# Kernel optimization log

Hardware: AMD Instinct MI355X
Metric: run time of the kernel (lower is better)

## Reference

```python
import jax, jax.numpy as jnp
import numpy as np

B, S, D, H = 4, 4096, 1024, 16
DH = D // H


def setup_inputs() -> dict:
    key = jax.random.key(0)
    ks = jax.random.split(key, 8)
    scale = 1.0 / np.sqrt(D)
    return {
        "q": jax.random.normal(ks[0], (B, S, D), jnp.float32),
        "k": jax.random.normal(ks[1], (B, S, D), jnp.float32),
        "v": jax.random.normal(ks[2], (B, S, D), jnp.float32),
        "mask": jax.random.uniform(ks[3], (H, H), jnp.float32),
        # torch nn.Linear weights, layout [out, in]; applied as x @ W.T
        "Wq": jax.random.normal(ks[4], (D, D), jnp.float32) * scale,
        "Wk": jax.random.normal(ks[5], (D, D), jnp.float32) * scale,
        "Wv": jax.random.normal(ks[6], (D, D), jnp.float32) * scale,
        "Wo": jax.random.normal(ks[7], (D, D), jnp.float32) * scale,
    }


def reference(q, k, v, mask, Wq, Wk, Wv, Wo):
    # projections (bias-free Linear): x @ W.T, then split to [B,S,H,DH]
    qh = (q @ Wq.T).reshape(B, S, H, DH)
    kh = (k @ Wk.T).reshape(B, S, H, DH)
    vh = (v @ Wv.T).reshape(B, S, H, DH)
    # Faithful to source: NO head/seq transpose, so attention is over the
    # head axis per token: score [B,S,H,H]
    score = jnp.einsum('bshd,bsgd->bshg', qh, kh) / np.sqrt(DH)
    score = score * mask  # multiplicative mask, broadcast [H,H]
    p = jax.nn.softmax(score, axis=-1)
    attn = jnp.einsum('bshg,bsgd->bshd', p, vh)  # [B,S,H,DH]
    out = attn.reshape(B, S, D) @ Wo.T
    return out
```

## Files before the change

### kernel.cpp

```cpp
#include <hip/hip_runtime.h>
#include <hip/hip_bf16.h>
#include <stdint.h>


namespace {
constexpr int kD  = 1024;
constexpr int kH  = 16;
constexpr int kDH = 64;
constexpr int kM  = 4 * 4096;
constexpr size_t PER = (size_t)kM * kD;
constexpr size_t WSZ = (size_t)kD * kD;

typedef __attribute__((ext_vector_type(4))) float f32x4;
typedef __attribute__((ext_vector_type(8))) short s16x8;

__device__ __forceinline__ unsigned short f2b(float f) {
  uint32_t x = __builtin_bit_cast(uint32_t, f);
  x += 0x7fffu + ((x >> 16) & 1u);
  return (unsigned short)(x >> 16);
}
__device__ __forceinline__ float b2f(unsigned short u) {
  return __builtin_bit_cast(float, (uint32_t)u << 16);
}

typedef __attribute__((address_space(3))) void as3_void;
typedef __attribute__((address_space(1))) void as1_void;
__device__ __forceinline__ void gload_lds16(const void* g, void* l) {
  __builtin_amdgcn_global_load_lds((const as1_void*)(uintptr_t)g,
                                   (as3_void*)(uint32_t)(uintptr_t)l, 16, 0, 0);
}

__global__ __launch_bounds__(256) void cvt_bf16(
    const float* __restrict__ q, const float* __restrict__ k, const float* __restrict__ v,
    const float* __restrict__ Wq, const float* __restrict__ Wk, const float* __restrict__ Wv,
    const float* __restrict__ Wo, unsigned short* __restrict__ out) {
  const size_t total8 = (3 * PER + 4 * WSZ) / 8;
  for (size_t i8 = (size_t)blockIdx.x * blockDim.x + threadIdx.x; i8 < total8;
       i8 += (size_t)gridDim.x * blockDim.x) {
    size_t i = i8 * 8;
    const float* s; size_t o;
    if (i < 3 * PER) {
      if (i < PER)            { s = q; o = i; }
      else if (i < 2 * PER)   { s = k; o = i - PER; }
      else                    { s = v; o = i - 2 * PER; }
    } else {
      size_t j = i - 3 * PER;
      if (j < WSZ)            { s = Wq; o = j; }
      else if (j < 2 * WSZ)   { s = Wk; o = j - WSZ; }
      else if (j < 3 * WSZ)   { s = Wv; o = j - 2 * WSZ; }
      else                    { s = Wo; o = j - 3 * WSZ; }
    }
    f32x4 f0 = ((const f32x4*)(s + o))[0];
    f32x4 f1 = ((const f32x4*)(s + o))[1];
    s16x8 r;
#pragma unroll
    for (int d = 0; d < 4; ++d) {
      r[d]     = (short)f2b(f0[d]);
      r[4 + d] = (short)f2b(f1[d]);
    }
    *(s16x8*)(out + i) = r;
  }
}

constexpr int BM2 = 256, BN2 = 256, BK2 = 64;
constexpr int KT2 = kD / BK2;

__device__ __forceinline__ void mfma16(f32x4 (&a)[2][4], s16x8 (&af)[2][2],
                                       s16x8 (&bw)[4][2]) {
  __builtin_amdgcn_s_setprio(1);
#pragma unroll
  for (int mi = 0; mi < 2; ++mi)
#pragma unroll
    for (int nj = 0; nj < 4; ++nj)
#pragma unroll
      for (int kk = 0; kk < 2; ++kk)
        a[mi][nj] = __builtin_amdgcn_mfma_f32_16x16x32_bf16(af[mi][kk], bw[nj][kk],
                                                            a[mi][nj], 0, 0, 0);
  __builtin_amdgcn_s_setprio(0);
}

template <bool OUT_F32>
__device__ __forceinline__ void gemmq_body(const unsigned short* __restrict__ A,
                                           const unsigned short* __restrict__ Bm,
                                           void* __restrict__ Cp) {
  constexpr int K = kD, N = kD;
  __shared__ __align__(16) unsigned short lds[65536];

  const int lin = blockIdx.y * gridDim.x + blockIdx.x;
  const int xcd = lin & 7;
  const int idx = lin >> 3;
  const int m0 = (xcd * 8 + (idx >> 2)) * BM2;
  const int n0 = (idx & 3) * BN2;

  const int t    = threadIdx.x;
  const int lane = t & 63;
  const int w    = t >> 6;
  const int wrow = w >> 1;
  const int wcol = w & 1;

  const int srow  = lane >> 3;
  const int sslot = (lane & 7) ^ srow;
  const int fr     = lane & 15;
  const int fkslot = lane >> 4;

  auto stageHalf = [&](const unsigned short* src, int grow0, int k0, int slot) {
    const unsigned short* g = src + (size_t)(grow0 + w * 16 + srow) * K + k0 + sslot * 8;
    unsigned short* l = lds + slot * 8192 + w * 16 * 64;
    gload_lds16(g, l);
    gload_lds16(g + (size_t)8 * K, l + 8 * 64);
  };
  auto rdA = [&](int slot, int mi, int kk) -> s16x8 {
    int r = wrow * 32 + mi * 16 + fr;
    int s16 = (kk * 4 + fkslot) ^ (r & 7);
    return *(const s16x8*)(lds + slot * 8192 + r * 64 + s16 * 8);
  };
  auto rdB = [&](int slot, int nj, int kk) -> s16x8 {
    int r = wcol * 64 + nj * 16 + fr;
    int s16 = (kk * 4 + fkslot) ^ (r & 7);
    return *(const s16x8*)(lds + slot * 8192 + r * 64 + s16 * 8);
  };

  f32x4 acc[4][2][4];
#pragma unroll
  for (int qi = 0; qi < 4; ++qi)
#pragma unroll
    for (int mi = 0; mi < 2; ++mi)
#pragma unroll
      for (int nj = 0; nj < 4; ++nj) acc[qi][mi][nj] = (f32x4){0.f, 0.f, 0.f, 0.f};

  stageHalf(A,  m0,       0, 0);
  stageHalf(Bm, n0,       0, 2);
  stageHalf(A,  m0 + 128, 0, 1);
  stageHalf(Bm, n0 + 128, 0, 3);

  s16x8 af[2][2], bw[4][2];

  for (int tt = 0; tt < KT2; ++tt) {
    const int b    = (tt & 1) * 4;
    const int nb   = b ^ 4;
    const int k1   = (tt + 1) * BK2;
    const bool more = (tt + 1 < KT2);

    asm volatile("s_waitcnt vmcnt(0)" ::: "memory");
    asm volatile("s_barrier" ::: "memory");
    if (more) { stageHalf(A, m0, k1, nb + 0); stageHalf(Bm, n0, k1, nb + 2); }
#pragma unroll
    for (int mi = 0; mi < 2; ++mi)
#pragma unroll
      for (int kk = 0; kk < 2; ++kk) af[mi][kk] = rdA(b + 0, mi, kk);
#pragma unroll
    for (int nj = 0; nj < 4; ++nj)
#pragma unroll
      for (int kk = 0; kk < 2; ++kk) bw[nj][kk] = rdB(b + 2, nj, kk);
    mfma16(acc[0], af, bw);

    asm volatile("s_barrier" ::: "memory");
    if (more) stageHalf(A, m0 + 128, k1, nb + 1);
#pragma unroll
    for (int mi = 0; mi < 2; ++mi)
#pragma unroll
      for (int kk = 0; kk < 2; ++kk) af[mi][kk] = rdA(b + 1, mi, kk);
    mfma16(acc[1], af, bw);

    asm volatile("s_barrier" ::: "memory");
    if (more) stageHalf(Bm, n0 + 128, k1, nb + 3);
#pragma unroll
    for (int nj = 0; nj < 4; ++nj)
#pragma unroll
      for (int kk = 0; kk < 2; ++kk) bw[nj][kk] = rdB(b + 3, nj, kk);
    mfma16(acc[2], af, bw);

    asm volatile("s_barrier" ::: "memory");
#pragma unroll
    for (int mi = 0; mi < 2; ++mi)
#pragma unroll
      for (int kk = 0; kk < 2; ++kk) af[mi][kk] = rdA(b + 0, mi, kk);
    mfma16(acc[3], af, bw);
  }

  constexpr int MH[4] = {0, 1, 1, 0};
  constexpr int NH[4] = {0, 0, 1, 1};
  const int cr = (lane >> 4) * 4;
  const int cc = lane & 15;
#pragma unroll
  for (int qi = 0; qi < 4; ++qi)
#pragma unroll
    for (int mi = 0; mi < 2; ++mi)
#pragma unroll
      for (int nj = 0; nj < 4; ++nj)
#pragma unroll
        for (int r = 0; r < 4; ++r) {
          size_t row = (size_t)(m0 + MH[qi] * 128 + wrow * 32 + mi * 16 + cr + r);
          size_t col = (size_t)(n0 + NH[qi] * 128 + wcol * 64 + nj * 16 + cc);
          if constexpr (OUT_F32)
            ((float*)Cp)[row * N + col] = acc[qi][mi][nj][r];
          else
            ((unsigned short*)Cp)[row * N + col] = f2b(acc[qi][mi][nj][r]);
        }
}

__global__ __launch_bounds__(512, 2) void proj_gemmq(
    const unsigned short* __restrict__ qb, const unsigned short* __restrict__ kb,
    const unsigned short* __restrict__ vb, const unsigned short* __restrict__ Wqb,
    const unsigned short* __restrict__ Wkb, const unsigned short* __restrict__ Wvb,
    unsigned short* __restrict__ qh, unsigned short* __restrict__ kh,
    unsigned short* __restrict__ vh) {
  const unsigned short *A, *W;
  unsigned short* C;
  if (blockIdx.z == 0)      { A = qb; W = Wqb; C = qh; }
  else if (blockIdx.z == 1) { A = kb; W = Wkb; C = kh; }
  else                      { A = vb; W = Wvb; C = vh; }
  gemmq_body<false>(A, W, C);
}

__global__ __launch_bounds__(512, 2) void out_gemmq(const unsigned short* __restrict__ attn,
                                                    const unsigned short* __restrict__ Wob,
                                                    float* __restrict__ out) {
  gemmq_body<true>(attn, Wob, out);
}

__global__ __launch_bounds__(256) void attn_tok(const unsigned short* __restrict__ qh,
                                                const unsigned short* __restrict__ kh,
                                                const unsigned short* __restrict__ vh,
                                                const float* __restrict__ mask,
                                                unsigned short* __restrict__ attn) {
  __shared__ float P[4][16][17];
  __shared__ __align__(16) unsigned short Vs[4][16 * 64];
  const int lane = threadIdx.x & 63;
  const int wid  = threadIdx.x >> 6;
  const size_t tok = (size_t)blockIdx.x * 4 + wid;

  const unsigned short* qp = qh + tok * kD;
  const unsigned short* kp = kh + tok * kD;
  const unsigned short* vp = vh + tok * kD;

  {
    const s16x8* src = (const s16x8*)vp;
    s16x8 a = src[2 * lane], b = src[2 * lane + 1];
    s16x8* dst = (s16x8*)Vs[wid];
    dst[2 * lane] = a;
    dst[2 * lane + 1] = b;
  }

  const int fr = lane & 15;
  const int fk = (lane >> 4) * 8;
  s16x8 a0 = *(const s16x8*)(qp + fr * kDH + fk);
  s16x8 a1 = *(const s16x8*)(qp + fr * kDH + 32 + fk);
  s16x8 b0 = *(const s16x8*)(kp + fr * kDH + fk);
  s16x8 b1 = *(const s16x8*)(kp + fr * kDH + 32 + fk);
  f32x4 s = {0.f, 0.f, 0.f, 0.f};
  s = __builtin_amdgcn_mfma_f32_16x16x32_bf16(a0, b0, s, 0, 0, 0);
  s = __builtin_amdgcn_mfma_f32_16x16x32_bf16(a1, b1, s, 0, 0, 0);

  const int cr = (lane >> 4) * 4;
  const int cc = lane & 15;
  float p[4];
#pragma unroll
  for (int r = 0; r < 4; ++r) {
    float val = s[r] * 0.125f * mask[(cr + r) * kH + cc];
    float mx = val;
#pragma unroll
    for (int d = 1; d < 16; d <<= 1) mx = fmaxf(mx, __shfl_xor(mx, d));
    float e = __expf(val - mx);
    float sum = e;
#pragma unroll
    for (int d = 1; d < 16; d <<= 1) sum += __shfl_xor(sum, d);
    p[r] = e / sum;
  }
#pragma unroll
  for (int r = 0; r < 4; ++r) P[wid][cr + r][cc] = p[r];

  const int h  = lane >> 2;
  const int d0 = (lane & 3) * 16;
  float o[16];
#pragma unroll
  for (int i = 0; i < 16; ++i) o[i] = 0.f;
#pragma unroll
  for (int g = 0; g < 16; ++g) {
    float pg = P[wid][h][g];
    s16x8 v0 = *(const s16x8*)(Vs[wid] + g * kDH + d0);
    s16x8 v1 = *(const s16x8*)(Vs[wid] + g * kDH + d0 + 8);
#pragma unroll
    for (int dd = 0; dd < 8; ++dd) {
      o[dd]     += pg * b2f((unsigned short)v0[dd]);
      o[8 + dd] += pg * b2f((unsigned short)v1[dd]);
    }
  }
  unsigned short* op = attn + tok * kD + h * kDH + d0;
  s16x8 r0, r1;
#pragma unroll
  for (int dd = 0; dd < 8; ++dd) {
    r0[dd] = (short)f2b(o[dd]);
    r1[dd] = (short)f2b(o[dd + 8]);
  }
  *(s16x8*)op = r0;
  *(s16x8*)(op + 8) = r1;
}

constexpr int BM = 128, BN = 128, BK = 32;
constexpr int LDSP = BK + 8;
__device__ __forceinline__ void cvt16_store(const float* __restrict__ g, short* __restrict__ l) {
  const f32x4* s4 = (const f32x4*)g;
  f32x4 f0 = s4[0], f1 = s4[1], f2 = s4[2], f3 = s4[3];
  s16x8 o0, o1;
#pragma unroll
  for (int i = 0; i < 4; ++i) {
    o0[i]     = (short)f2b(f0[i]);
    o0[4 + i] = (short)f2b(f1[i]);
    o1[i]     = (short)f2b(f2[i]);
    o1[4 + i] = (short)f2b(f3[i]);
  }
  *(s16x8*)l = o0;
  *(s16x8*)(l + 8) = o1;
}

template <bool A_BF16, bool OUT_F32>
__device__ __forceinline__ void gemm_body_cvt(const void* __restrict__ Ap,
                                              const float* __restrict__ Wp,
                                              void* __restrict__ Cp) {
  constexpr int N = kD, K = kD;
  __shared__ short As[BM * LDSP];
  __shared__ short Bs[BN * LDSP];
  const int t  = threadIdx.x;
  const int m0 = blockIdx.y * BM;
  const int n0 = blockIdx.x * BN;
  const int srow = t >> 1;
  const int scol = (t & 1) * 16;
  const int lane = t & 63;
  const int wid  = t >> 6;
  const int wm   = (wid >> 1) * 64;
  const int wn   = (wid & 1) * 64;
  const int fr   = lane & 15;
  const int fk   = (lane >> 4) * 8;

  f32x4 acc[4][4];
#pragma unroll
  for (int i = 0; i < 4; ++i)
#pragma unroll
    for (int j = 0; j < 4; ++j) acc[i][j] = (f32x4){0.f, 0.f, 0.f, 0.f};

  for (int k0 = 0; k0 < K; k0 += BK) {
    if constexpr (A_BF16) {
      const unsigned short* Ab = (const unsigned short*)Ap;
      const s16x8* src = (const s16x8*)(Ab + (size_t)(m0 + srow) * K + k0 + scol);
      s16x8 v0 = src[0], v1 = src[1];
      *(s16x8*)(As + srow * LDSP + scol) = v0;
      *(s16x8*)(As + srow * LDSP + scol + 8) = v1;
    } else {
      cvt16_store((const float*)Ap + (size_t)(m0 + srow) * K + k0 + scol,
                  As + srow * LDSP + scol);
    }
    cvt16_store(Wp + (size_t)(n0 + srow) * K + k0 + scol, Bs + srow * LDSP + scol);
    __syncthreads();
    s16x8 af[4], bw[4];
#pragma unroll
    for (int i = 0; i < 4; ++i)
      af[i] = *(const s16x8*)(As + (wm + i * 16 + fr) * LDSP + fk);
#pragma unroll
    for (int j = 0; j < 4; ++j)
      bw[j] = *(const s16x8*)(Bs + (wn + j * 16 + fr) * LDSP + fk);
#pragma unroll
    for (int i = 0; i < 4; ++i)
#pragma unroll
      for (int j = 0; j < 4; ++j)
        acc[i][j] = __builtin_amdgcn_mfma_f32_16x16x32_bf16(af[i], bw[j], acc[i][j], 0, 0, 0);
    __syncthreads();
  }
  const int cr = (lane >> 4) * 4;
  const int cc = lane & 15;
#pragma unroll
  for (int i = 0; i < 4; ++i)
#pragma unroll
    for (int j = 0; j < 4; ++j)
#pragma unroll
      for (int r = 0; r < 4; ++r) {
        size_t row = (size_t)(m0 + wm + i * 16 + cr + r);
        size_t col = (size_t)(n0 + wn + j * 16 + cc);
        if constexpr (OUT_F32)
          ((float*)Cp)[row * N + col] = acc[i][j][r];
        else
          ((unsigned short*)Cp)[row * N + col] = f2b(acc[i][j][r]);
      }
}

__global__ __launch_bounds__(256) void proj_gemm_cvt(
    const float* __restrict__ q, const float* __restrict__ k, const float* __restrict__ v,
    const float* __restrict__ Wq, const float* __restrict__ Wk, const float* __restrict__ Wv,
    unsigned short* __restrict__ qh, unsigned short* __restrict__ kh,
    unsigned short* __restrict__ vh) {
  const float* A; const float* W; unsigned short* C;
  if (blockIdx.z == 0)      { A = q; W = Wq; C = qh; }
  else if (blockIdx.z == 1) { A = k; W = Wk; C = kh; }
  else                      { A = v; W = Wv; C = vh; }
  gemm_body_cvt<false, false>(A, W, C);
}

__global__ __launch_bounds__(256) void out_gemm_cvt(const unsigned short* __restrict__ attn,
                                                    const float* __restrict__ Wo,
                                                    float* __restrict__ out) {
  gemm_body_cvt<true, true>(attn, Wo, out);
}

}

extern "C" void kernel_launch(void* const* d_in, const int* in_sizes, int n_in,
                              void* d_out, int out_size, void* d_ws, size_t ws_size,
                              hipStream_t stream) {
  (void)in_sizes; (void)n_in; (void)out_size;
  const float* q    = (const float*)d_in[0];
  const float* k    = (const float*)d_in[1];
  const float* v    = (const float*)d_in[2];
  const float* mask = (const float*)d_in[3];
  const float* Wq   = (const float*)d_in[4];
  const float* Wk   = (const float*)d_in[5];
  const float* Wv   = (const float*)d_in[6];
  const float* Wo   = (const float*)d_in[7];

  const size_t need = (6 * PER + 4 * WSZ) * sizeof(unsigned short);
  if (ws_size >= need) {
    unsigned short* qb  = (unsigned short*)d_ws;
    unsigned short* kb  = qb + PER;
    unsigned short* vb  = kb + PER;
    unsigned short* Wqb = vb + PER;
    unsigned short* Wkb = Wqb + WSZ;
    unsigned short* Wvb = Wkb + WSZ;
    unsigned short* Wob = Wvb + WSZ;
    unsigned short* qh  = Wob + WSZ;
    unsigned short* kh  = qh + PER;
    unsigned short* vh  = kh + PER;
    unsigned short* at  = qb;

    cvt_bf16<<<2048, 256, 0, stream>>>(q, k, v, Wq, Wk, Wv, Wo, qb);
    proj_gemmq<<<dim3(kD / BN2, kM / BM2, 3), 512, 0, stream>>>(qb, kb, vb, Wqb, Wkb, Wvb,
                                                                qh, kh, vh);
    attn_tok<<<dim3(kM / 4), 256, 0, stream>>>(qh, kh, vh, mask, at);
    out_gemmq<<<dim3(kD / BN2, kM / BM2), 512, 0, stream>>>(at, Wob, (float*)d_out);
  } else {
    unsigned short* qh = (unsigned short*)d_ws;
    unsigned short* kh = qh + PER;
    unsigned short* vh = kh + PER;
    unsigned short* at = (ws_size >= 4 * PER * sizeof(unsigned short)) ? (vh + PER) : qh;
    proj_gemm_cvt<<<dim3(kD / BN, kM / BM, 3), 256, 0, stream>>>(q, k, v, Wq, Wk, Wv,
                                                                 qh, kh, vh);
    attn_tok<<<dim3(kM / 4), 256, 0, stream>>>(qh, kh, vh, mask, at);
    out_gemm_cvt<<<dim3(kD / BN, kM / BM), 256, 0, stream>>>(at, Wo, (float*)d_out);
  }
}
```

Before: 227.8 us.

## Fuse fp32-to-bf16 activation conversion into projection GEMM A-tile staging

Removes the separate pass that converted q, k and v to bf16. The projection GEMM now loads fp32 A tiles into registers, converts them, and writes them swizzled into LDS, interleaved with the existing barrier phases; only the weights are still pre-converted, by a smaller kernel. This drops a large read-and-write pass over the activations and shrinks the workspace, and the attention output now reuses the qh buffer. The cost is that A staging moves from direct global-to-LDS loads to a register path, with more VGPR pressure, more global traffic per tile from fp32 rereads across column blocks, and an extra lgkmcnt wait per iteration.

```diff
diff --git a/kernel.cpp b/kernel.cpp
--- a/kernel.cpp
+++ b/kernel.cpp
@@ -30,26 +30,19 @@
                                    (as3_void*)(uint32_t)(uintptr_t)l, 16, 0, 0);
 }
 
-__global__ __launch_bounds__(256) void cvt_bf16(
-    const float* __restrict__ q, const float* __restrict__ k, const float* __restrict__ v,
-    const float* __restrict__ Wq, const float* __restrict__ Wk, const float* __restrict__ Wv,
-    const float* __restrict__ Wo, unsigned short* __restrict__ out) {
-  const size_t total8 = (3 * PER + 4 * WSZ) / 8;
+__global__ __launch_bounds__(256) void cvt_w(
+    const float* __restrict__ Wq, const float* __restrict__ Wk,
+    const float* __restrict__ Wv, const float* __restrict__ Wo,
+    unsigned short* __restrict__ out) {
+  const size_t total8 = 4 * WSZ / 8;
   for (size_t i8 = (size_t)blockIdx.x * blockDim.x + threadIdx.x; i8 < total8;
        i8 += (size_t)gridDim.x * blockDim.x) {
     size_t i = i8 * 8;
     const float* s; size_t o;
-    if (i < 3 * PER) {
-      if (i < PER)            { s = q; o = i; }
-      else if (i < 2 * PER)   { s = k; o = i - PER; }
-      else                    { s = v; o = i - 2 * PER; }
-    } else {
-      size_t j = i - 3 * PER;
-      if (j < WSZ)            { s = Wq; o = j; }
-      else if (j < 2 * WSZ)   { s = Wk; o = j - WSZ; }
-      else if (j < 3 * WSZ)   { s = Wv; o = j - 2 * WSZ; }
-      else                    { s = Wo; o = j - 3 * WSZ; }
-    }
+    if (i < WSZ)            { s = Wq; o = i; }
+    else if (i < 2 * WSZ)   { s = Wk; o = i - WSZ; }
+    else if (i < 3 * WSZ)   { s = Wv; o = i - 2 * WSZ; }
+    else                    { s = Wo; o = i - 3 * WSZ; }
     f32x4 f0 = ((const f32x4*)(s + o))[0];
     f32x4 f1 = ((const f32x4*)(s + o))[1];
     s16x8 r;
@@ -79,8 +72,8 @@
   __builtin_amdgcn_s_setprio(0);
 }
 
-template <bool OUT_F32>
-__device__ __forceinline__ void gemmq_body(const unsigned short* __restrict__ A,
+template <bool A_F32, bool OUT_F32>
+__device__ __forceinline__ void gemmq_body(const void* __restrict__ Ap,
                                            const unsigned short* __restrict__ Bm,
                                            void* __restrict__ Cp) {
   constexpr int K = kD, N = kD;
@@ -103,11 +96,37 @@
   const int fr     = lane & 15;
   const int fkslot = lane >> 4;
 
+  const unsigned short* Ab = (const unsigned short*)Ap;
+  const float*          Af = (const float*)Ap;
+
   auto stageHalf = [&](const unsigned short* src, int grow0, int k0, int slot) {
     const unsigned short* g = src + (size_t)(grow0 + w * 16 + srow) * K + k0 + sslot * 8;
     unsigned short* l = lds + slot * 8192 + w * 16 * 64;
     gload_lds16(g, l);
     gload_lds16(g + (size_t)8 * K, l + 8 * 64);
+  };
+  auto loadAf32 = [&](int grow0, int k0, f32x4 (&ar)[4]) {
+#pragma unroll
+    for (int i = 0; i < 2; ++i) {
+      const float* src =
+          Af + (size_t)(grow0 + w * 16 + i * 8 + (lane >> 3)) * K + k0 + (lane & 7) * 8;
+      ar[2 * i]     = ((const f32x4*)src)[0];
+      ar[2 * i + 1] = ((const f32x4*)src)[1];
+    }
+  };
+  auto cvtWriteA = [&](int slot, f32x4 (&ar)[4]) {
+#pragma unroll
+    for (int i = 0; i < 2; ++i) {
+      const int rl = w * 16 + i * 8 + (lane >> 3);
+      const int sl = (lane & 7) ^ (rl & 7);
+      s16x8 c;
+#pragma unroll
+      for (int d = 0; d < 4; ++d) {
+        c[d]     = (short)f2b(ar[2 * i][d]);
+        c[4 + d] = (short)f2b(ar[2 * i + 1][d]);
+      }
+      *(s16x8*)(lds + slot * 8192 + rl * 64 + sl * 8) = c;
+    }
   };
   auto rdA = [&](int slot, int mi, int kk) -> s16x8 {
     int r = wrow * 32 + mi * 16 + fr;
@@ -128,10 +147,20 @@
 #pragma unroll
       for (int nj = 0; nj < 4; ++nj) acc[qi][mi][nj] = (f32x4){0.f, 0.f, 0.f, 0.f};
 
-  stageHalf(A,  m0,       0, 0);
-  stageHalf(Bm, n0,       0, 2);
-  stageHalf(A,  m0 + 128, 0, 1);
-  stageHalf(Bm, n0 + 128, 0, 3);
+  f32x4 ar[4];
+
+  if constexpr (A_F32) {
+    stageHalf(Bm, n0,       0, 2);
+    stageHalf(Bm, n0 + 128, 0, 3);
+    loadAf32(m0,       0, ar); cvtWriteA(0, ar);
+    asm volatile("" ::: "memory");
+    loadAf32(m0 + 128, 0, ar); cvtWriteA(1, ar);
+  } else {
+    stageHalf(Ab, m0,       0, 0);
+    stageHalf(Bm, n0,       0, 2);
+    stageHalf(Ab, m0 + 128, 0, 1);
+    stageHalf(Bm, n0 + 128, 0, 3);
+  }
 
   s16x8 af[2][2], bw[4][2];
 
@@ -141,9 +170,13 @@
     const int k1   = (tt + 1) * BK2;
     const bool more = (tt + 1 < KT2);
 
-    asm volatile("s_waitcnt vmcnt(0)" ::: "memory");
+    asm volatile("s_waitcnt vmcnt(0) lgkmcnt(0)" ::: "memory");
     asm volatile("s_barrier" ::: "memory");
-    if (more) { stageHalf(A, m0, k1, nb + 0); stageHalf(Bm, n0, k1, nb + 2); }
+    if (more) {
+      if constexpr (A_F32) { loadAf32(m0, k1, ar); }
+      else                 { stageHalf(Ab, m0, k1, nb + 0); }
+      stageHalf(Bm, n0, k1, nb + 2);
+    }
 #pragma unroll
     for (int mi = 0; mi < 2; ++mi)
 #pragma unroll
@@ -155,7 +188,15 @@
     mfma16(acc[0], af, bw);
 
     asm volatile("s_barrier" ::: "memory");
-    if (more) stageHalf(A, m0 + 128, k1, nb + 1);
+    if (more) {
+      if constexpr (A_F32) {
+        cvtWriteA(nb + 0, ar);
+        asm volatile("" ::: "memory");
+        loadAf32(m0 + 128, k1, ar);
+      } else {
+        stageHalf(Ab, m0 + 128, k1, nb + 1);
+      }
+    }
 #pragma unroll
     for (int mi = 0; mi < 2; ++mi)
 #pragma unroll
@@ -171,6 +212,9 @@
     mfma16(acc[2], af, bw);
 
     asm volatile("s_barrier" ::: "memory");
+    if (more) {
+      if constexpr (A_F32) cvtWriteA(nb + 1, ar);
+    }
 #pragma unroll
     for (int mi = 0; mi < 2; ++mi)
 #pragma unroll
@@ -200,23 +244,23 @@
 }
 
 __global__ __launch_bounds__(512, 2) void proj_gemmq(
-    const unsigned short* __restrict__ qb, const unsigned short* __restrict__ kb,
-    const unsigned short* __restrict__ vb, const unsigned short* __restrict__ Wqb,
-    const unsigned short* __restrict__ Wkb, const unsigned short* __restrict__ Wvb,
-    unsigned short* __restrict__ qh, unsigned short* __restrict__ kh,
-    unsigned short* __restrict__ vh) {
-  const unsigned short *A, *W;
+    const float* __restrict__ q, const float* __restrict__ k, const float* __restrict__ v,
+    const unsigned short* __restrict__ Wqb, const unsigned short* __restrict__ Wkb,
+    const unsigned short* __restrict__ Wvb, unsigned short* __restrict__ qh,
+    unsigned short* __restrict__ kh, unsigned short* __restrict__ vh) {
+  const float* A;
+  const unsigned short* W;
   unsigned short* C;
-  if (blockIdx.z == 0)      { A = qb; W = Wqb; C = qh; }
-  else if (blockIdx.z == 1) { A = kb; W = Wkb; C = kh; }
-  else                      { A = vb; W = Wvb; C = vh; }
-  gemmq_body<false>(A, W, C);
+  if (blockIdx.z == 0)      { A = q; W = Wqb; C = qh; }
+  else if (blockIdx.z == 1) { A = k; W = Wkb; C = kh; }
+  else                      { A = v; W = Wvb; C = vh; }
+  gemmq_body<true, false>(A, W, C);
 }
 
 __global__ __launch_bounds__(512, 2) void out_gemmq(const unsigned short* __restrict__ attn,
                                                     const unsigned short* __restrict__ Wob,
                                                     float* __restrict__ out) {
-  gemmq_body<true>(attn, Wob, out);
+  gemmq_body<false, true>(attn, Wob, out);
 }
 
 __global__ __launch_bounds__(256) void attn_tok(const unsigned short* __restrict__ qh,
@@ -416,22 +460,19 @@
   const float* Wv   = (const float*)d_in[6];
   const float* Wo   = (const float*)d_in[7];
 
-  const size_t need = (6 * PER + 4 * WSZ) * sizeof(unsigned short);
+  const size_t need = (3 * PER + 4 * WSZ) * sizeof(unsigned short);
   if (ws_size >= need) {
-    unsigned short* qb  = (unsigned short*)d_ws;
-    unsigned short* kb  = qb + PER;
-    unsigned short* vb  = kb + PER;
-    unsigned short* Wqb = vb + PER;
+    unsigned short* Wqb = (unsigned short*)d_ws;
     unsigned short* Wkb = Wqb + WSZ;
     unsigned short* Wvb = Wkb + WSZ;
     unsigned short* Wob = Wvb + WSZ;
     unsigned short* qh  = Wob + WSZ;
     unsigned short* kh  = qh + PER;
     unsigned short* vh  = kh + PER;
-    unsigned short* at  = qb;
-
-    cvt_bf16<<<2048, 256, 0, stream>>>(q, k, v, Wq, Wk, Wv, Wo, qb);
-    proj_gemmq<<<dim3(kD / BN2, kM / BM2, 3), 512, 0, stream>>>(qb, kb, vb, Wqb, Wkb, Wvb,
+    unsigned short* at  = qh;
+
+    cvt_w<<<256, 256, 0, stream>>>(Wq, Wk, Wv, Wo, Wqb);
+    proj_gemmq<<<dim3(kD / BN2, kM / BM2, 3), 512, 0, stream>>>(q, k, v, Wqb, Wkb, Wvb,
                                                                 qh, kh, vh);
     attn_tok<<<dim3(kM / 4), 256, 0, stream>>>(qh, kh, vh, mask, at);
     out_gemmq<<<dim3(kD / BN2, kM / BM2), 512, 0, stream>>>(at, Wob, (float*)d_out);
```

Result: slower. 238.1 us (+4.5%).
